# Performance work log

Hardware: AMD Instinct MI355X
Metric: run time of the kernel (lower is better)

Reference implementation:

```python
import jax, jax.numpy as jnp
import numpy as np

H = 16
D_MODEL = 1024
B, S = 2, 2048
DH = D_MODEL // H


def setup_inputs() -> dict:
    key = jax.random.key(0)
    ks = jax.random.split(key, 12)
    std = 0.02
    q = jax.random.normal(ks[0], (B, S, D_MODEL), dtype=jnp.float32)
    k = jax.random.normal(ks[1], (B, S, D_MODEL), dtype=jnp.float32)
    v = jax.random.normal(ks[2], (B, S, D_MODEL), dtype=jnp.float32)
    # additive causal mask: 0 on/below diagonal, -1e9 above
    causal = jnp.tril(jnp.ones((S, S), dtype=bool))
    mask = jnp.where(causal, 0.0, -1e9).astype(jnp.float32)[None, None, :, :]
    def dense(kk):
        return (jax.random.normal(kk, (D_MODEL, D_MODEL), dtype=jnp.float32) * std,
                jnp.zeros((D_MODEL,), dtype=jnp.float32))
    Wq, bq = dense(ks[3])
    Wk, bk = dense(ks[4])
    Wv, bv = dense(ks[5])
    Wo, bo = dense(ks[6])
    return {"q": q, "k": k, "v": v, "mask": mask,
            "Wq": Wq, "bq": bq, "Wk": Wk, "bk": bk,
            "Wv": Wv, "bv": bv, "Wo": Wo, "bo": bo}


def reference(q, k, v, mask, Wq, bq, Wk, bk, Wv, bv, Wo, bo):
    b, s, d = q.shape
    def split_heads(x):  # [b,s,d] -> [b,h,s,dh]
        return x.reshape(b, s, H, DH).transpose(0, 2, 1, 3)
    qh = split_heads(q @ Wq + bq)
    kh = split_heads(k @ Wk + bk)
    vh = split_heads(v @ Wv + bv)
    scale = 1.0 / jnp.sqrt(jnp.asarray(DH, dtype=qh.dtype))
    scores = jnp.einsum('bhqd,bhkd->bhqk', qh, kh) * scale + mask
    weights = jax.nn.softmax(scores, axis=-1)
    ctx = jnp.einsum('bhqk,bhkd->bhqd', weights, vh)
    ctx = ctx.transpose(0, 2, 1, 3).reshape(b, s, d)
    return ctx @ Wo + bo
```

## Files before the change

kernel.cpp:

```cpp
#include <hip/hip_runtime.h>
#include <hip/hip_bf16.h>
#include <stdint.h>

typedef __bf16 bf16x8 __attribute__((ext_vector_type(8)));
typedef float  f32x4  __attribute__((ext_vector_type(4)));
typedef __hip_bfloat16 bf16_t;

#define D_MODEL 1024
#define NH 16
#define DH 64
#define BB 2
#define SS 2048
#define MTOT (BB*SS)
#define NQT (SS/64)

#define GBM 128
#define GBN 64
#define GBK 64

__global__ void cvt_qkv_kernel(const float* __restrict__ q, const float* __restrict__ k,
                               const float* __restrict__ v, bf16_t* __restrict__ dst) {
  const int n1v = MTOT * D_MODEL / 4;
  int tid = blockIdx.x * blockDim.x + threadIdx.x;
  int stride = gridDim.x * blockDim.x;
  for (int i = tid; i < 3 * n1v; i += stride) {
    int which = i / n1v;
    int j = i - which * n1v;
    const float4* src = (const float4*)(which == 0 ? q : (which == 1 ? k : v));
    float4 f = src[j];
    union { bf16_t h[4]; short4 s4; } u;
    u.h[0] = __float2bfloat16(f.x);
    u.h[1] = __float2bfloat16(f.y);
    u.h[2] = __float2bfloat16(f.z);
    u.h[3] = __float2bfloat16(f.w);
    ((short4*)dst)[(size_t)which * n1v + j] = u.s4;
  }
}

__global__ void transpose_w_kernel(const float* __restrict__ W0, const float* __restrict__ W1,
                                   const float* __restrict__ W2, const float* __restrict__ W3,
                                   bf16_t* __restrict__ WtAll) {
  __shared__ float tile[32][33];
  const int z = blockIdx.z;
  const float* W = (z == 0) ? W0 : (z == 1) ? W1 : (z == 2) ? W2 : W3;
  bf16_t* Wt = WtAll + (size_t)z * D_MODEL * D_MODEL;
  const int tx = threadIdx.x, ty = threadIdx.y;
  const int bx = blockIdx.x, by = blockIdx.y;
#pragma unroll
  for (int i = 0; i < 4; ++i)
    tile[ty + i * 8][tx] = W[(size_t)(by * 32 + ty + i * 8) * D_MODEL + bx * 32 + tx];
  __syncthreads();
#pragma unroll
  for (int i = 0; i < 4; ++i)
    Wt[(size_t)(bx * 32 + ty + i * 8) * D_MODEL + by * 32 + tx] =
        __float2bfloat16(tile[tx][ty + i * 8]);
}

__device__ __forceinline__ void g2lds16(const bf16_t* g, bf16_t* l) {
  __builtin_amdgcn_global_load_lds((__attribute__((address_space(1))) void*)(g),
                                   (__attribute__((address_space(3))) void*)(l), 16, 0, 0);
}

__device__ __forceinline__ void gemm_tile_mainloop(const bf16_t* __restrict__ A,
                                                   const bf16_t* __restrict__ Bt,
                                                   bf16_t* As, bf16_t* Bs,
                                                   int m0, int n0, f32x4 acc[4][2]) {
  const int tid = threadIdx.x;
  const int wv = tid >> 6, ln = tid & 63;
  const int wr = wv >> 1, wc = wv & 1;
  const int lr = ln & 15, lg = ln >> 4;

#pragma unroll
  for (int mi = 0; mi < 4; ++mi)
#pragma unroll
    for (int ni = 0; ni < 2; ++ni)
      acc[mi][ni] = (f32x4){0.f, 0.f, 0.f, 0.f};

  for (int kt = 0; kt < D_MODEL / GBK; ++kt) {
#pragma unroll
    for (int c = 0; c < 6; ++c) {
      int chunk = wv * 6 + c;
      int row8 = ln >> 3;
      int col = (ln & 7) * 8;
      if (chunk < 16) {
        g2lds16(A  + (size_t)(m0 + chunk * 8 + row8) * D_MODEL + kt * GBK + col,
                As + chunk * 8 * GBK);
      } else {
        g2lds16(Bt + (size_t)(n0 + (chunk - 16) * 8 + row8) * D_MODEL + kt * GBK + col,
                Bs + (chunk - 16) * 8 * GBK);
      }
    }
    __syncthreads();
#pragma unroll
    for (int ks = 0; ks < 2; ++ks) {
      bf16x8 af[4], bfr[2];
#pragma unroll
      for (int mi = 0; mi < 4; ++mi)
        af[mi] = *(const bf16x8*)(As + (size_t)(wr * 64 + mi * 16 + lr) * GBK + ks * 32 + lg * 8);
#pragma unroll
      for (int ni = 0; ni < 2; ++ni)
        bfr[ni] = *(const bf16x8*)(Bs + (size_t)(wc * 32 + ni * 16 + lr) * GBK + ks * 32 + lg * 8);
#pragma unroll
      for (int mi = 0; mi < 4; ++mi)
#pragma unroll
        for (int ni = 0; ni < 2; ++ni)
          acc[mi][ni] = __builtin_amdgcn_mfma_f32_16x16x32_bf16(af[mi], bfr[ni], acc[mi][ni], 0, 0, 0);
    }
    __syncthreads();
  }
}

__global__ __launch_bounds__(256)
void qk_proj_kernel(const bf16_t* __restrict__ Aq, const bf16_t* __restrict__ Ak,
                    const bf16_t* __restrict__ WtAll,
                    const float* __restrict__ bq, const float* __restrict__ bk,
                    bf16_t* __restrict__ Qg, bf16_t* __restrict__ Kg) {
  __shared__ bf16_t As[GBM * GBK];
  __shared__ bf16_t Bs[GBN * GBK];
  const int z = blockIdx.z;
  const bf16_t* A = (z == 0) ? Aq : Ak;
  const bf16_t* Bt = WtAll + (size_t)z * D_MODEL * D_MODEL;
  const float* bias = (z == 0) ? bq : bk;
  bf16_t* Out = (z == 0) ? Qg : Kg;
  const float scale = (z == 0) ? 0.125f : 1.0f;
  const int m0 = blockIdx.y * GBM, n0 = blockIdx.x * GBN;

  f32x4 acc[4][2];
  gemm_tile_mainloop(A, Bt, As, Bs, m0, n0, acc);

  const int tid = threadIdx.x;
  const int wv = tid >> 6, ln = tid & 63;
  const int wr = wv >> 1, wc = wv & 1;
  const int lr = ln & 15, lg = ln >> 4;

#pragma unroll
  for (int mi = 0; mi < 4; ++mi) {
#pragma unroll
    for (int ni = 0; ni < 2; ++ni) {
      int ncol = n0 + wc * 32 + ni * 16 + lr;
      float bsv = bias[ncol];
#pragma unroll
      for (int j = 0; j < 4; ++j) {
        int mrow = m0 + wr * 64 + mi * 16 + lg * 4 + j;
        Out[(size_t)mrow * D_MODEL + ncol] = __float2bfloat16((acc[mi][ni][j] + bsv) * scale);
      }
    }
  }
}

__global__ __launch_bounds__(256)
void vt_proj_kernel(const bf16_t* __restrict__ Wtv, const bf16_t* __restrict__ Av,
                    const float* __restrict__ bv, bf16_t* __restrict__ Vt) {
  __shared__ bf16_t As[GBM * GBK];
  __shared__ bf16_t Bs[GBN * GBK];
  const int m0 = blockIdx.y * GBM, n0 = blockIdx.x * GBN;

  f32x4 acc[4][2];
  gemm_tile_mainloop(Wtv, Av, As, Bs, m0, n0, acc);

  const int tid = threadIdx.x;
  const int wv = tid >> 6, ln = tid & 63;
  const int wr = wv >> 1, wc = wv & 1;
  const int lr = ln & 15, lg = ln >> 4;

#pragma unroll
  for (int mi = 0; mi < 4; ++mi) {
#pragma unroll
    for (int ni = 0; ni < 2; ++ni) {
      int ncol = n0 + wc * 32 + ni * 16 + lr;
#pragma unroll
      for (int j = 0; j < 4; ++j) {
        int mrow = m0 + wr * 64 + mi * 16 + lg * 4 + j;
        Vt[(size_t)mrow * MTOT + ncol] = __float2bfloat16(acc[mi][ni][j] + bv[mrow]);
      }
    }
  }
}

__global__ __launch_bounds__(256)
void out_gemm_kernel(const bf16_t* __restrict__ Ctx, const bf16_t* __restrict__ Wto,
                     const float* __restrict__ bo, float* __restrict__ out) {
  __shared__ bf16_t As[GBM * GBK];
  __shared__ bf16_t Bs[GBN * GBK];
  const int m0 = blockIdx.y * GBM, n0 = blockIdx.x * GBN;

  f32x4 acc[4][2];
  gemm_tile_mainloop(Ctx, Wto, As, Bs, m0, n0, acc);

  const int tid = threadIdx.x;
  const int wv = tid >> 6, ln = tid & 63;
  const int wr = wv >> 1, wc = wv & 1;
  const int lr = ln & 15, lg = ln >> 4;

#pragma unroll
  for (int mi = 0; mi < 4; ++mi) {
#pragma unroll
    for (int ni = 0; ni < 2; ++ni) {
      int ncol = n0 + wc * 32 + ni * 16 + lr;
      float bsv = bo[ncol];
#pragma unroll
      for (int j = 0; j < 4; ++j) {
        int mrow = m0 + wr * 64 + mi * 16 + lg * 4 + j;
        out[(size_t)mrow * D_MODEL + ncol] = acc[mi][ni][j] + bsv;
      }
    }
  }
}

__device__ __forceinline__ uint32_t pack2bf(float a, float b) {
  union { __hip_bfloat16 h; unsigned short u; } ua, ub;
  ua.h = __float2bfloat16(a);
  ub.h = __float2bfloat16(b);
  return (uint32_t)ua.u | ((uint32_t)ub.u << 16);
}

#define PSTRIDE 44

__device__ __forceinline__ void attn_run(
    f32x4 acc_o[2][4], f32x4 acc_l[2], float m_run[2],
    const bf16x8 qf[2][2], const bf16_t* Kbase, const bf16_t* Vbase,
    uint32_t (*P32)[PSTRIDE], int q0, int t0, int t1, int lr, int lg, bf16x8 onesf) {
  bf16x8 kf_cur[2][4];
#pragma unroll
  for (int ks = 0; ks < 2; ++ks)
#pragma unroll
    for (int kb = 0; kb < 4; ++kb)
      kf_cur[ks][kb] = *(const bf16x8*)(Kbase + (size_t)(t0 * 64 + kb * 16 + lr) * D_MODEL + ks * 32 + lg * 8);

  for (int t = t0; t < t1; ++t) {
    const int kv0 = t * 64;
    f32x4 sc[2][4];
#pragma unroll
    for (int qi = 0; qi < 2; ++qi)
#pragma unroll
      for (int kb = 0; kb < 4; ++kb) sc[qi][kb] = (f32x4){0.f, 0.f, 0.f, 0.f};

    __builtin_amdgcn_s_setprio(1);
#pragma unroll
    for (int ks = 0; ks < 2; ++ks) {
#pragma unroll
      for (int kb = 0; kb < 4; ++kb) {
        sc[0][kb] = __builtin_amdgcn_mfma_f32_16x16x32_bf16(kf_cur[ks][kb], qf[0][ks], sc[0][kb], 0, 0, 0);
        sc[1][kb] = __builtin_amdgcn_mfma_f32_16x16x32_bf16(kf_cur[ks][kb], qf[1][ks], sc[1][kb], 0, 0, 0);
      }
    }
    __builtin_amdgcn_s_setprio(0);

    bf16x8 kf_nxt[2][4];
    if (t + 1 < t1) {
#pragma unroll
      for (int ks = 0; ks < 2; ++ks)
#pragma unroll
        for (int kb = 0; kb < 4; ++kb)
          kf_nxt[ks][kb] = *(const bf16x8*)(Kbase + (size_t)(kv0 + 64 + kb * 16 + lr) * D_MODEL + ks * 32 + lg * 8);
    }
    bf16x8 vf[2][4];
#pragma unroll
    for (int ks = 0; ks < 2; ++ks)
#pragma unroll
      for (int db = 0; db < 4; ++db)
        vf[ks][db] = *(const bf16x8*)(Vbase + (size_t)(db * 16 + lr) * MTOT + kv0 + ks * 32 + lg * 8);

    if (kv0 + 63 > q0) {
#pragma unroll
      for (int qi = 0; qi < 2; ++qi) {
        int qc = q0 + qi * 16 + lr;
#pragma unroll
        for (int kb = 0; kb < 4; ++kb)
#pragma unroll
          for (int r = 0; r < 4; ++r) {
            int kc = kv0 + kb * 16 + 4 * lg + r;
            if (kc > qc) sc[qi][kb][r] = -1e30f;
          }
      }
    }

#pragma unroll
    for (int qi = 0; qi < 2; ++qi) {
      float vm = sc[qi][0][0];
#pragma unroll
      for (int kb = 0; kb < 4; ++kb)
#pragma unroll
        for (int r = 0; r < 4; ++r) vm = fmaxf(vm, sc[qi][kb][r]);
      vm = fmaxf(vm, __shfl_xor(vm, 16, 64));
      vm = fmaxf(vm, __shfl_xor(vm, 32, 64));
      float mo = m_run[qi];
      float mn = fmaxf(mo, vm);
      float scl = __expf(mo - mn);
      m_run[qi] = mn;
#pragma unroll
      for (int kb = 0; kb < 4; ++kb)
#pragma unroll
        for (int hh = 0; hh < 2; ++hh) {
          float p0 = __expf(sc[qi][kb][2 * hh]     - mn);
          float p1 = __expf(sc[qi][kb][2 * hh + 1] - mn);
          P32[qi * 16 + lr][8 * kb + 2 * lg + hh] = pack2bf(p0, p1);
        }
#pragma unroll
      for (int r = 0; r < 4; ++r) acc_l[qi][r] *= scl;
#pragma unroll
      for (int db = 0; db < 4; ++db)
#pragma unroll
        for (int r = 0; r < 4; ++r) acc_o[qi][db][r] *= scl;
    }

    asm volatile("s_waitcnt lgkmcnt(0)" ::: "memory");
    __builtin_amdgcn_sched_barrier(0);

    bf16x8 pb[2][2];
#pragma unroll
    for (int qi = 0; qi < 2; ++qi)
#pragma unroll
      for (int ks = 0; ks < 2; ++ks)
        pb[qi][ks] = *(const bf16x8*)&P32[qi * 16 + lr][16 * ks + 4 * lg];

    __builtin_amdgcn_s_setprio(1);
#pragma unroll
    for (int ks = 0; ks < 2; ++ks) {
#pragma unroll
      for (int qi = 0; qi < 2; ++qi) {
        acc_l[qi] = __builtin_amdgcn_mfma_f32_16x16x32_bf16(onesf, pb[qi][ks], acc_l[qi], 0, 0, 0);
#pragma unroll
        for (int db = 0; db < 4; ++db)
          acc_o[qi][db] = __builtin_amdgcn_mfma_f32_16x16x32_bf16(vf[ks][db], pb[qi][ks], acc_o[qi][db], 0, 0, 0);
      }
    }
    __builtin_amdgcn_s_setprio(0);

    if (t + 1 < t1) {
#pragma unroll
      for (int ks = 0; ks < 2; ++ks)
#pragma unroll
        for (int kb = 0; kb < 4; ++kb)
          kf_cur[ks][kb] = kf_nxt[ks][kb];
    }
  }
}

__device__ __forceinline__ void attn_load_q(bf16x8 qf[2][2], const bf16_t* Qbase,
                                            int q0, int lr, int lg) {
#pragma unroll
  for (int qi = 0; qi < 2; ++qi)
#pragma unroll
    for (int ks = 0; ks < 2; ++ks)
      qf[qi][ks] = *(const bf16x8*)(Qbase + (size_t)(q0 + qi * 16 + lr) * D_MODEL + ks * 32 + lg * 8);
}

__device__ __forceinline__ void attn_init(f32x4 acc_o[2][4], f32x4 acc_l[2], float m_run[2]) {
#pragma unroll
  for (int qi = 0; qi < 2; ++qi) {
#pragma unroll
    for (int db = 0; db < 4; ++db) acc_o[qi][db] = (f32x4){0.f, 0.f, 0.f, 0.f};
    acc_l[qi] = (f32x4){0.f, 0.f, 0.f, 0.f};
    m_run[qi] = -1e30f;
  }
}

__device__ __forceinline__ void store_ctx_tile(
    uint32_t (*P32)[PSTRIDE], const f32x4 acc_o[2][4], const f32x4 acc_l[2],
    bf16_t* __restrict__ Ctx, int b, int h, int q0, int ln, int lr, int lg) {
#pragma unroll
  for (int qi = 0; qi < 2; ++qi) {
    float rl = 1.0f / acc_l[qi][0];
#pragma unroll
    for (int db = 0; db < 4; ++db)
#pragma unroll
      for (int hh = 0; hh < 2; ++hh)
        P32[qi * 16 + lr][8 * db + 2 * lg + hh] =
            pack2bf(acc_o[qi][db][2 * hh] * rl, acc_o[qi][db][2 * hh + 1] * rl);
  }
  asm volatile("s_waitcnt lgkmcnt(0)" ::: "memory");
  __builtin_amdgcn_sched_barrier(0);
#pragma unroll
  for (int c = 0; c < 4; ++c) {
    int row = (ln >> 2) + 16 * (c >> 1);
    int dwc = (ln & 3) * 4 + 16 * (c & 1);
    bf16x8 v = *(const bf16x8*)&P32[row][dwc];
    *(bf16x8*)(Ctx + (size_t)(b * SS + q0 + row) * D_MODEL + h * DH + dwc * 2) = v;
  }
}

__global__ __launch_bounds__(256)
void attn_kernel(const bf16_t* __restrict__ Qg, const bf16_t* __restrict__ Kg,
                 const bf16_t* __restrict__ Vt, bf16_t* __restrict__ Ctx) {
  __shared__ __align__(16) uint32_t P32[4][32][PSTRIDE];
  __shared__ __align__(16) float O_part[2][32][68];
  __shared__ float ml_part[2][32][2];
  const int bh = blockIdx.x;
  const int pp = blockIdx.y;
  const int b = bh >> 4, h = bh & 15;
  const int wv = threadIdx.x >> 6, ln = threadIdx.x & 63;
  const int lr = ln & 15, lg = ln >> 4;

  const int qt_lo = pp, qt_hi = NQT - 1 - pp;
  const int h0 = 16 - pp;
  const int rh = wv & 1;

  const size_t qkbase = (size_t)b * SS * D_MODEL + (size_t)h * DH;
  const bf16_t* Qbase = Qg + qkbase;
  const bf16_t* Kbase = Kg + qkbase;
  const bf16_t* Vbase = Vt + (size_t)(h * DH) * MTOT + b * SS;

  bf16x8 onesf;
#pragma unroll
  for (int j = 0; j < 8; ++j) onesf[j] = (__bf16)1.0f;

  bf16x8 qf[2][2];
  f32x4 acc_o[2][4];
  f32x4 acc_l[2];
  float m_run[2];
  const int q0_hi = qt_hi * 64 + rh * 32;

  if (wv < 2) {
    const int q0_lo = qt_lo * 64 + rh * 32;
    attn_load_q(qf, Qbase, q0_lo, lr, lg);
    attn_init(acc_o, acc_l, m_run);
    attn_run(acc_o, acc_l, m_run, qf, Kbase, Vbase, P32[wv], q0_lo, 0, pp + 1, lr, lg, onesf);
    store_ctx_tile(P32[wv], acc_o, acc_l, Ctx, b, h, q0_lo, ln, lr, lg);

    attn_load_q(qf, Qbase, q0_hi, lr, lg);
    attn_init(acc_o, acc_l, m_run);
    attn_run(acc_o, acc_l, m_run, qf, Kbase, Vbase, P32[wv], q0_hi, 0, h0, lr, lg, onesf);
  } else {
    attn_load_q(qf, Qbase, q0_hi, lr, lg);
    attn_init(acc_o, acc_l, m_run);
    attn_run(acc_o, acc_l, m_run, qf, Kbase, Vbase, P32[wv], q0_hi, h0, NQT - pp, lr, lg, onesf);
    const int pidx = wv - 2;
#pragma unroll
    for (int qi = 0; qi < 2; ++qi) {
#pragma unroll
      for (int db = 0; db < 4; ++db)
        *(f32x4*)&O_part[pidx][qi * 16 + lr][16 * db + 4 * lg] = acc_o[qi][db];
      if (lg == 0) {
        ml_part[pidx][qi * 16 + lr][0] = m_run[qi];
        ml_part[pidx][qi * 16 + lr][1] = acc_l[qi][0];
      }
    }
  }

  __syncthreads();

  if (wv < 2) {
#pragma unroll
    for (int qi = 0; qi < 2; ++qi) {
      float m1 = m_run[qi];
      float m2 = ml_part[wv][qi * 16 + lr][0];
      float mn = fmaxf(m1, m2);
      float a1 = __expf(m1 - mn);
      float a2 = __expf(m2 - mn);
      float l = a1 * acc_l[qi][0] + a2 * ml_part[wv][qi * 16 + lr][1];
#pragma unroll
      for (int db = 0; db < 4; ++db) {
        f32x4 po = *(const f32x4*)&O_part[wv][qi * 16 + lr][16 * db + 4 * lg];
#pragma unroll
        for (int r = 0; r < 4; ++r)
          acc_o[qi][db][r] = a1 * acc_o[qi][db][r] + a2 * po[r];
      }
      acc_l[qi] = (f32x4){l, l, l, l};
    }
    store_ctx_tile(P32[wv], acc_o, acc_l, Ctx, b, h, q0_hi, ln, lr, lg);
  }
}

extern "C" void kernel_launch(void* const* d_in, const int* in_sizes, int n_in,
                              void* d_out, int out_size, void* d_ws, size_t ws_size,
                              hipStream_t stream) {
  const float* q  = (const float*)d_in[0];
  const float* k  = (const float*)d_in[1];
  const float* v  = (const float*)d_in[2];
  const float* bq = (const float*)d_in[5];
  const float* bk = (const float*)d_in[7];
  const float* bv = (const float*)d_in[9];
  const float* bo = (const float*)d_in[11];
  const float* Wq = (const float*)d_in[4];
  const float* Wk = (const float*)d_in[6];
  const float* Wv = (const float*)d_in[8];
  const float* Wo = (const float*)d_in[10];
  float* out = (float*)d_out;

  char* w = (char*)d_ws;
  bf16_t* Aqkv  = (bf16_t*)(w);
  bf16_t* WtAll = (bf16_t*)(w + 25165824);
  bf16_t* Qg    = (bf16_t*)(w + 33554432);
  bf16_t* Kg    = (bf16_t*)(w + 41943040);
  bf16_t* Vt    = (bf16_t*)(w + 50331648);
  bf16_t* Ctx   = (bf16_t*)(w + 58720256);

  cvt_qkv_kernel<<<2048, 256, 0, stream>>>(q, k, v, Aqkv);
  transpose_w_kernel<<<dim3(32, 32, 4), dim3(32, 8), 0, stream>>>(Wq, Wk, Wv, Wo, WtAll);
  qk_proj_kernel<<<dim3(16, 32, 2), 256, 0, stream>>>(
      Aqkv, Aqkv + (size_t)MTOT * D_MODEL, WtAll, bq, bk, Qg, Kg);
  vt_proj_kernel<<<dim3(64, 8), 256, 0, stream>>>(
      WtAll + 2 * (size_t)D_MODEL * D_MODEL, Aqkv + 2 * (size_t)MTOT * D_MODEL, bv, Vt);
  attn_kernel<<<dim3(32, 16), 256, 0, stream>>>(Qg, Kg, Vt, Ctx);
  out_gemm_kernel<<<dim3(16, 32), 256, 0, stream>>>(
      Ctx, WtAll + 3 * (size_t)D_MODEL * D_MODEL, bo, out);
}
```

Baseline: 280.7 us.

## Double-buffer LDS tiles in projection GEMM mainloop to overlap loads with MFMA

The GEMM mainloop now keeps two LDS buffers for the A and B tiles. It issues the global-to-LDS loads for the next k-tile before computing on the current one, so memory latency can overlap with MFMA work, and it drops one barrier per iteration. The cost is twice the shared memory per block (48KB), which may lower occupancy. The overlap is limited because the barrier at the end of each iteration still waits for the prefetch to finish.

```diff
diff --git a/kernel.cpp b/kernel.cpp
--- a/kernel.cpp
+++ b/kernel.cpp
@@ -61,6 +61,25 @@
                                    (__attribute__((address_space(3))) void*)(l), 16, 0, 0);
 }
 
+__device__ __forceinline__ void gemm_stage(const bf16_t* __restrict__ A,
+                                           const bf16_t* __restrict__ Bt,
+                                           bf16_t* As, bf16_t* Bs,
+                                           int m0, int n0, int kt, int wv, int ln) {
+  const int row8 = ln >> 3;
+  const int col = (ln & 7) * 8;
+#pragma unroll
+  for (int c = 0; c < 6; ++c) {
+    int chunk = wv * 6 + c;
+    if (chunk < 16) {
+      g2lds16(A + (size_t)(m0 + chunk * 8 + row8) * D_MODEL + kt * GBK + col,
+              As + chunk * 8 * GBK);
+    } else {
+      g2lds16(Bt + (size_t)(n0 + (chunk - 16) * 8 + row8) * D_MODEL + kt * GBK + col,
+              Bs + (chunk - 16) * 8 * GBK);
+    }
+  }
+}
+
 __device__ __forceinline__ void gemm_tile_mainloop(const bf16_t* __restrict__ A,
                                                    const bf16_t* __restrict__ Bt,
                                                    bf16_t* As, bf16_t* Bs,
@@ -76,30 +95,26 @@
     for (int ni = 0; ni < 2; ++ni)
       acc[mi][ni] = (f32x4){0.f, 0.f, 0.f, 0.f};
 
-  for (int kt = 0; kt < D_MODEL / GBK; ++kt) {
-#pragma unroll
-    for (int c = 0; c < 6; ++c) {
-      int chunk = wv * 6 + c;
-      int row8 = ln >> 3;
-      int col = (ln & 7) * 8;
-      if (chunk < 16) {
-        g2lds16(A  + (size_t)(m0 + chunk * 8 + row8) * D_MODEL + kt * GBK + col,
-                As + chunk * 8 * GBK);
-      } else {
-        g2lds16(Bt + (size_t)(n0 + (chunk - 16) * 8 + row8) * D_MODEL + kt * GBK + col,
-                Bs + (chunk - 16) * 8 * GBK);
-      }
-    }
-    __syncthreads();
+  const int NT = D_MODEL / GBK;
+  gemm_stage(A, Bt, As, Bs, m0, n0, 0, wv, ln);
+  __syncthreads();
+
+  int cur = 0;
+  for (int kt = 0; kt < NT; ++kt) {
+    if (kt + 1 < NT)
+      gemm_stage(A, Bt, As + (cur ^ 1) * (GBM * GBK), Bs + (cur ^ 1) * (GBN * GBK),
+                 m0, n0, kt + 1, wv, ln);
+    const bf16_t* Ab = As + cur * (GBM * GBK);
+    const bf16_t* Bb = Bs + cur * (GBN * GBK);
 #pragma unroll
     for (int ks = 0; ks < 2; ++ks) {
       bf16x8 af[4], bfr[2];
 #pragma unroll
       for (int mi = 0; mi < 4; ++mi)
-        af[mi] = *(const bf16x8*)(As + (size_t)(wr * 64 + mi * 16 + lr) * GBK + ks * 32 + lg * 8);
+        af[mi] = *(const bf16x8*)(Ab + (size_t)(wr * 64 + mi * 16 + lr) * GBK + ks * 32 + lg * 8);
 #pragma unroll
       for (int ni = 0; ni < 2; ++ni)
-        bfr[ni] = *(const bf16x8*)(Bs + (size_t)(wc * 32 + ni * 16 + lr) * GBK + ks * 32 + lg * 8);
+        bfr[ni] = *(const bf16x8*)(Bb + (size_t)(wc * 32 + ni * 16 + lr) * GBK + ks * 32 + lg * 8);
 #pragma unroll
       for (int mi = 0; mi < 4; ++mi)
 #pragma unroll
@@ -107,6 +122,7 @@
           acc[mi][ni] = __builtin_amdgcn_mfma_f32_16x16x32_bf16(af[mi], bfr[ni], acc[mi][ni], 0, 0, 0);
     }
     __syncthreads();
+    cur ^= 1;
   }
 }
 
@@ -115,8 +131,8 @@
                     const bf16_t* __restrict__ WtAll,
                     const float* __restrict__ bq, const float* __restrict__ bk,
                     bf16_t* __restrict__ Qg, bf16_t* __restrict__ Kg) {
-  __shared__ bf16_t As[GBM * GBK];
-  __shared__ bf16_t Bs[GBN * GBK];
+  __shared__ bf16_t As[2 * GBM * GBK];
+  __shared__ bf16_t Bs[2 * GBN * GBK];
   const int z = blockIdx.z;
   const bf16_t* A = (z == 0) ? Aq : Ak;
   const bf16_t* Bt = WtAll + (size_t)z * D_MODEL * D_MODEL;
@@ -151,8 +167,8 @@
 __global__ __launch_bounds__(256)
 void vt_proj_kernel(const bf16_t* __restrict__ Wtv, const bf16_t* __restrict__ Av,
                     const float* __restrict__ bv, bf16_t* __restrict__ Vt) {
-  __shared__ bf16_t As[GBM * GBK];
-  __shared__ bf16_t Bs[GBN * GBK];
+  __shared__ bf16_t As[2 * GBM * GBK];
+  __shared__ bf16_t Bs[2 * GBN * GBK];
   const int m0 = blockIdx.y * GBM, n0 = blockIdx.x * GBN;
 
   f32x4 acc[4][2];
@@ -180,8 +196,8 @@
 __global__ __launch_bounds__(256)
 void out_gemm_kernel(const bf16_t* __restrict__ Ctx, const bf16_t* __restrict__ Wto,
                      const float* __restrict__ bo, float* __restrict__ out) {
-  __shared__ bf16_t As[GBM * GBK];
-  __shared__ bf16_t Bs[GBN * GBK];
+  __shared__ bf16_t As[2 * GBM * GBK];
+  __shared__ bf16_t Bs[2 * GBN * GBK];
   const int m0 = blockIdx.y * GBM, n0 = blockIdx.x * GBN;
 
   f32x4 acc[4][2];
```

Measured after the change: 264.7 us. -5.7%, faster.
